# Kernel tuning notes

Measured on AMD Instinct MI355X. Metric: run time of the kernel, lower is better.

Reference implementation:

```python
import jax, jax.numpy as jnp
import numpy as np

B, C, N, Hdim, Wdim = 32, 64, 16384, 128, 128  # N = Hdim*Wdim, C = dim = num_embeddings
EPS = 1e-5


def setup_inputs() -> dict:
    key = jax.random.key(0)
    ks = jax.random.split(key, 6)
    s = 0.05  # weight scale
    return {
        "x": jax.random.normal(ks[0], (B, C, N), dtype=jnp.float32),
        "Wq": jax.random.normal(ks[1], (C, C), dtype=jnp.float32) * s,   # Conv1d q (1x1)
        "bq": jnp.zeros((C,), jnp.float32),
        "gamma": jnp.ones((C,), jnp.float32),                              # BatchNorm1d affine
        "beta": jnp.zeros((C,), jnp.float32),
        "Wq2": jax.random.normal(ks[2], (C, C), dtype=jnp.float32) * s,  # Conv1d q2 (1x1)
        "bq2": jnp.zeros((C,), jnp.float32),
        "Wsr": jax.random.normal(ks[3], (C, C), dtype=jnp.float32) * s,  # Conv2d sr, k=1,s=1 -> 1x1
        "bsr": jnp.zeros((C,), jnp.float32),
        "Wc": jax.random.normal(ks[4], (C, C), dtype=jnp.float32) * s,   # Conv1d conv (1x1, no bias)
        "H": Hdim,
        "W": Wdim,
    }


def reference(x, Wq, bq, gamma, beta, Wq2, bq2, Wsr, bsr, Wc, H, W):
    # x: (B, C, N), N = H*W, sr_ratio = 1
    # q = q2(BN(q(x))) -- all 1x1 convs; BN uses batch statistics (torch training mode)
    q = jnp.einsum('oc,bcn->bon', Wq, x) + bq[None, :, None]            # (B,C,N)
    mu = q.mean(axis=(0, 2), keepdims=True)
    var = q.var(axis=(0, 2), keepdims=True)
    q = (q - mu) * jax.lax.rsqrt(var + EPS)
    q = q * gamma[None, :, None] + beta[None, :, None]
    q = jnp.einsum('oc,bcn->bon', Wq2, q) + bq2[None, :, None]          # (B,C,N)

    # k = sr(x) with kernel/stride 1 -> 1x1 conv, then permute to (B,N,C)
    k = jnp.einsum('oc,bcn->bon', Wsr, x) + bsr[None, :, None]          # (B,C,N)

    # v = AvgPool1d(C) over the channel axis of x^T -> channel mean, (B,1,N)
    v = x.mean(axis=1, keepdims=True)                                    # (B,1,N)

    # attn = q @ k^T over the N axis -> (B,C,C), then MaxPool1d(C) -> row-wise max (B,C,1)
    attn = jnp.einsum('bcn,bdn->bcd', q, k)                              # (B,C,C)
    attn = attn.max(axis=-1, keepdims=True)                              # (B,C,1)

    # out = conv( attn @ v )  -- outer product broadcast, then 1x1 conv (no bias)
    out = attn * v                                                       # (B,C,N)
    out = jnp.einsum('oc,bcn->bon', Wc, out)                             # (B,C,N)
    return out
```

## Files before the change

### kernel.cpp

```cpp
#include <hip/hip_runtime.h>
#include <hip/hip_bf16.h>

#define B_ 32
#define C_ 64
#define N_ 16384
constexpr float BN_INV = 1.0f / (32.0f * 16384.0f);

typedef float f32x4 __attribute__((ext_vector_type(4)));
typedef short s16x8 __attribute__((ext_vector_type(8)));

constexpr size_t WS_GPART = 0;
constexpr size_t WS_RPART = WS_GPART + (size_t)512 * 4096;
constexpr size_t WS_G     = WS_RPART + (size_t)512 * 64;
constexpr size_t WS_RB    = WS_G + (size_t)32 * 4096;
constexpr size_t WS_V     = WS_RB + (size_t)32 * 64;
constexpr size_t WS_W     = WS_V + (size_t)32 * N_;

__device__ constexpr int P1I[10] = {0,0,0,0,1,1,1,2,2,3};
__device__ constexpr int P1J[10] = {0,1,2,3,1,2,3,2,3,3};
__device__ constexpr int P1AT[4][4] = {{0,1,2,3},{1,4,5,6},{2,5,7,8},{3,6,8,9}};

__device__ __forceinline__ unsigned short bf16_rne_s(float f) {
    unsigned u = __float_as_uint(f);
    unsigned r = u + 0x7FFFu + ((u >> 16) & 1u);
    return (unsigned short)(r >> 16);
}
__device__ __forceinline__ unsigned cvt_pk_bf16(float lo, float hi) {
    unsigned r;
    asm("v_cvt_pk_bf16_f32 %0, %1, %2" : "=v"(r) : "v"(lo), "v"(hi));
    return r;
}
__device__ __forceinline__ void cvt8hi(const f32x4& a, const f32x4& b, s16x8& hi) {
    union { unsigned w[4]; s16x8 v; } u;
    u.w[0] = cvt_pk_bf16(a[0], a[1]);
    u.w[1] = cvt_pk_bf16(a[2], a[3]);
    u.w[2] = cvt_pk_bf16(b[0], b[1]);
    u.w[3] = cvt_pk_bf16(b[2], b[3]);
    hi = u.v;
}

__global__ __launch_bounds__(512, 2) void k1(const float* __restrict__ x, float* __restrict__ ws) {
    __shared__ __align__(16) float rawb[4][10 * 256];
    __shared__ float rws[8][64];
    const int t = threadIdx.x, wv = t >> 6, lane = t & 63;
    const int b = blockIdx.x >> 4, ch = blockIdx.x & 15;
    const int kg = lane >> 4, cl = lane & 15;
    const float* xb = x + ((size_t)b * C_ + cl) * N_ + ch * 1024 + kg * 8;

    f32x4 accP1[10];
    #pragma unroll
    for (int i = 0; i < 10; ++i) accP1[i] = (f32x4){0.f, 0.f, 0.f, 0.f};
    f32x4 rs = {0.f, 0.f, 0.f, 0.f};

    f32x4 cA[4], cB[4], nA[4], nB[4];
    #pragma unroll
    for (int g = 0; g < 4; ++g) {
        cA[g] = *(const f32x4*)(xb + (size_t)g * (16 * N_) + wv * 32);
        cB[g] = *(const f32x4*)(xb + (size_t)g * (16 * N_) + wv * 32 + 4);
    }

    for (int w = 0; w < 4; ++w) {
        if (w < 3) {
            const int noff = (8 * (w + 1) + wv) * 32;
            #pragma unroll
            for (int g = 0; g < 4; ++g) {
                nA[g] = *(const f32x4*)(xb + (size_t)g * (16 * N_) + noff);
                nB[g] = *(const f32x4*)(xb + (size_t)g * (16 * N_) + noff + 4);
            }
        }
        s16x8 hi[4];
        #pragma unroll
        for (int g = 0; g < 4; ++g) cvt8hi(cA[g], cB[g], hi[g]);

        f32x4 s0 = cA[0] + cA[1] + cA[2] + cA[3];
        f32x4 s1 = cB[0] + cB[1] + cB[2] + cB[3];
        #pragma unroll
        for (int m = 1; m <= 8; m <<= 1) {
            #pragma unroll
            for (int j = 0; j < 4; ++j) {
                s0[j] += __shfl_xor(s0[j], m);
                s1[j] += __shfl_xor(s1[j], m);
            }
        }
        if (cl == 0) {
            float* vp = ws + WS_V + (size_t)b * N_ + ch * 1024 + (8 * w + wv) * 32 + kg * 8;
            *(f32x4*)vp       = s0 * 0.015625f;
            *(f32x4*)(vp + 4) = s1 * 0.015625f;
        }
        #pragma unroll
        for (int g = 0; g < 4; ++g)
            rs[g] += cA[g][0] + cA[g][1] + cA[g][2] + cA[g][3]
                   + cB[g][0] + cB[g][1] + cB[g][2] + cB[g][3];

        #pragma unroll
        for (int i = 0; i < 10; ++i)
            accP1[i] = __builtin_amdgcn_mfma_f32_16x16x32_bf16(hi[P1I[i]], hi[P1J[i]], accP1[i], 0, 0, 0);

        #pragma unroll
        for (int g = 0; g < 4; ++g) { cA[g] = nA[g]; cB[g] = nB[g]; }
    }

    #pragma unroll
    for (int g = 0; g < 4; ++g) {
        rs[g] += __shfl_xor(rs[g], 16);
        rs[g] += __shfl_xor(rs[g], 32);
    }
    if (lane < 16) {
        #pragma unroll
        for (int g = 0; g < 4; ++g) rws[wv][g * 16 + lane] = rs[g];
    }

    if (wv < 4) {
        float* dst = rawb[wv];
        #pragma unroll
        for (int i = 0; i < 10; ++i) *(f32x4*)(dst + i * 256 + lane * 4) = accP1[i];
    }
    __syncthreads();
    if (wv >= 4) {
        float* dst = rawb[wv - 4];
        #pragma unroll
        for (int i = 0; i < 10; ++i) {
            f32x4 o = *(f32x4*)(dst + i * 256 + lane * 4);
            *(f32x4*)(dst + i * 256 + lane * 4) = o + accP1[i];
        }
    }
    __syncthreads();
    if (t < 64) {
        float s = 0.f;
        #pragma unroll
        for (int g = 0; g < 8; ++g) s += rws[g][t];
        ws[WS_RPART + (size_t)blockIdx.x * 64 + t] = s;
    }
    float* gp = ws + WS_GPART + (size_t)blockIdx.x * 4096;
    for (int e = t; e < 4096; e += 512) {
        const int r = e >> 6, c = e & 63;
        const int bi = r >> 4, bj = c >> 4, rr = r & 15, cc = c & 15;
        const int i1 = P1AT[bi][bj] * 256;
        const int o1 = (bi <= bj) ? (((rr >> 2) * 16 + cc) * 4 + (rr & 3))
                                  : (((cc >> 2) * 16 + rr) * 4 + (cc & 3));
        gp[e] = rawb[0][i1 + o1] + rawb[1][i1 + o1] + rawb[2][i1 + o1] + rawb[3][i1 + o1];
    }
}

__global__ __launch_bounds__(256) void k2a(float* __restrict__ ws) {
    const int b = blockIdx.x >> 3, sl = blockIdx.x & 7, t = threadIdx.x;
    #pragma unroll
    for (int h = 0; h < 2; ++h) {
        const int e = sl * 512 + h * 256 + t;
        float s = 0.f;
        for (int chn = 0; chn < 16; ++chn) s += ws[WS_GPART + ((size_t)(b * 16 + chn)) * 4096 + e];
        ws[WS_G + (size_t)b * 4096 + e] = s;
    }
    if (sl == 0 && t < 64) {
        float s = 0.f;
        for (int chn = 0; chn < 16; ++chn) s += ws[WS_RPART + (size_t)(b * 16 + chn) * 64 + t];
        ws[WS_RB + b * 64 + t] = s;
    }
}

__global__ __launch_bounds__(256) void k2b(const float* __restrict__ Wq, const float* __restrict__ gamma,
                                           const float* __restrict__ beta, const float* __restrict__ Wq2,
                                           const float* __restrict__ bq2, const float* __restrict__ Wsr,
                                           const float* __restrict__ bsr, const float* __restrict__ Wc,
                                           float* __restrict__ ws) {
    __shared__ __align__(16) unsigned short OPH[3][64 * 72];
    __shared__ float F1[64 * 65], F2[64 * 65];
    __shared__ float mS[64], muS[64], DS[64], abv[64], quadS[64];
    __shared__ float rl[64], ul[64], avs[64], sbv[64], pls[64], aml[64];
    const int bb = blockIdx.x, t = threadIdx.x;
    const int w = t >> 6, lane = t & 63, cl = lane & 15, jg = lane >> 4;
    const int sr = t >> 2, sc0 = (t & 3) * 16;

    {
        f32x4 s[4];
        #pragma unroll
        for (int j = 0; j < 4; ++j) s[j] = (f32x4){0.f, 0.f, 0.f, 0.f};
        for (int b = 0; b < 32; ++b) {
            const float* gbp = ws + WS_G + (size_t)b * 4096 + sr * 64 + sc0;
            #pragma unroll
            for (int j = 0; j < 4; ++j) s[j] += *(const f32x4*)(gbp + 4 * j);
        }
        s16x8 h8[2];
        #pragma unroll
        for (int q = 0; q < 2; ++q)
            #pragma unroll
            for (int j = 0; j < 8; ++j)
                h8[q][j] = (short)bf16_rne_s(s[q * 2 + (j >> 2)][j & 3] * BN_INV);
        *(s16x8*)(&OPH[0][sr * 72 + sc0])     = h8[0];
        *(s16x8*)(&OPH[0][sr * 72 + sc0 + 8]) = h8[1];
    }
    #pragma unroll
    for (int mtx = 0; mtx < 2; ++mtx) {
        const float* src = (mtx == 0 ? Wq : Wq2) + sr * 64 + sc0;
        float* F = (mtx == 0) ? F1 : F2;
        s16x8 h8[2];
        #pragma unroll
        for (int q = 0; q < 2; ++q) {
            f32x4 a = *(const f32x4*)(src + q * 8);
            f32x4 b = *(const f32x4*)(src + q * 8 + 4);
            #pragma unroll
            for (int j = 0; j < 8; ++j) {
                float v = (j < 4) ? a[j] : b[j - 4];
                F[sr * 65 + sc0 + q * 8 + j] = v;
                h8[q][j] = (short)bf16_rne_s(v);
            }
        }
        unsigned short* H = OPH[1 + mtx];
        *(s16x8*)(&H[sr * 72 + sc0])     = h8[0];
        *(s16x8*)(&H[sr * 72 + sc0 + 8]) = h8[1];
    }
    if (t < 64) {
        float sm = 0.f;
        for (int b = 0; b < 32; ++b) sm += ws[WS_RB + b * 64 + t];
        mS[t] = sm * BN_INV;
        rl[t] = ws[WS_RB + bb * 64 + t];
        sbv[t] = bsr[t];
    }
    __syncthreads();

    auto mm64 = [&](const unsigned short* AH, const unsigned short* BH, f32x4 acc[4]) {
        #pragma unroll
        for (int ks = 0; ks < 2; ++ks) {
            const int ko = ks * 32 + jg * 8;
            s16x8 ah = *(const s16x8*)(AH + (16 * w + cl) * 72 + ko);
            #pragma unroll
            for (int bj = 0; bj < 4; ++bj) {
                s16x8 bh = *(const s16x8*)(BH + (16 * bj + cl) * 72 + ko);
                acc[bj] = __builtin_amdgcn_mfma_f32_16x16x32_bf16(ah, bh, acc[bj], 0, 0, 0);
            }
        }
    };

    {
        f32x4 acc[4];
        #pragma unroll
        for (int i = 0; i < 4; ++i) acc[i] = (f32x4){0.f, 0.f, 0.f, 0.f};
        mm64(OPH[1], OPH[0], acc);
        float s[4] = {0.f, 0.f, 0.f, 0.f};
        #pragma unroll
        for (int j = 0; j < 4; ++j) {
            const int row = 16 * w + jg * 4 + j;
            #pragma unroll
            for (int bj = 0; bj < 4; ++bj) s[j] += acc[bj][j] * F1[row * 65 + 16 * bj + cl];
        }
        #pragma unroll
        for (int m = 1; m <= 8; m <<= 1)
            #pragma unroll
            for (int j = 0; j < 4; ++j) s[j] += __shfl_xor(s[j], m);
        if (cl == 0) {
            #pragma unroll
            for (int j = 0; j < 4; ++j) quadS[16 * w + jg * 4 + j] = s[j];
        }
        if (t < 64) {
            float s2 = 0.f;
            for (int c = 0; c < 64; ++c) s2 += F1[t * 65 + c] * mS[c];
            muS[t] = s2;
        }
    }
    __syncthreads();

    if (t < 64) {
        const float var = quadS[t] - muS[t] * muS[t];
        const float D = gamma[t] * rsqrtf(var + 1e-5f);
        DS[t] = D;
        abv[t] = beta[t] - D * muS[t];
    }
    __syncthreads();
    {
        s16x8 h8[2];
        #pragma unroll
        for (int q = 0; q < 2; ++q)
            #pragma unroll
            for (int j = 0; j < 8; ++j) {
                const int c = sc0 + q * 8 + j;
                h8[q][j] = (short)bf16_rne_s(DS[c] * F1[c * 65 + sr]);
            }
        *(s16x8*)(&OPH[0][sr * 72 + sc0])     = h8[0];
        *(s16x8*)(&OPH[0][sr * 72 + sc0 + 8]) = h8[1];
    }
    if (t < 64) {
        float s = 0.f;
        for (int k = 0; k < 64; ++k) s += F2[t * 65 + k] * abv[k];
        avs[t] = s + bq2[t];
    }
    __syncthreads();

    {
        f32x4 acc[4];
        #pragma unroll
        for (int i = 0; i < 4; ++i) acc[i] = (f32x4){0.f, 0.f, 0.f, 0.f};
        mm64(OPH[2], OPH[0], acc);
        float s[4] = {0.f, 0.f, 0.f, 0.f};
        #pragma unroll
        for (int bj = 0; bj < 4; ++bj) {
            const float cv = rl[16 * bj + cl];
            #pragma unroll
            for (int j = 0; j < 4; ++j) s[j] += acc[bj][j] * cv;
        }
        #pragma unroll
        for (int m = 1; m <= 8; m <<= 1)
            #pragma unroll
            for (int j = 0; j < 4; ++j) s[j] += __shfl_xor(s[j], m);
        if (cl == 0) {
            #pragma unroll
            for (int j = 0; j < 4; ++j) ul[16 * w + jg * 4 + j] = s[j];
        }
        #pragma unroll
        for (int bj = 0; bj < 4; ++bj)
            #pragma unroll
            for (int j = 0; j < 4; ++j) {
                const int row = 16 * w + jg * 4 + j, col = 16 * bj + cl;
                OPH[1][row * 72 + col] = (unsigned short)bf16_rne_s(acc[bj][j]);
            }
    }
    __syncthreads();

    {
        const float* gbp = ws + WS_G + (size_t)bb * 4096 + sr * 64 + sc0;
        s16x8 h8[2];
        #pragma unroll
        for (int q = 0; q < 2; ++q) {
            f32x4 a = *(const f32x4*)(gbp + q * 8);
            f32x4 b = *(const f32x4*)(gbp + q * 8 + 4);
            #pragma unroll
            for (int j = 0; j < 8; ++j)
                h8[q][j] = (short)bf16_rne_s((j < 4) ? a[j] : b[j - 4]);
        }
        *(s16x8*)(&OPH[0][sr * 72 + sc0])     = h8[0];
        *(s16x8*)(&OPH[0][sr * 72 + sc0 + 8]) = h8[1];
        const float* ssrc = Wsr + sr * 64 + sc0;
        #pragma unroll
        for (int q = 0; q < 2; ++q) {
            f32x4 a = *(const f32x4*)(ssrc + q * 8);
            f32x4 b = *(const f32x4*)(ssrc + q * 8 + 4);
            #pragma unroll
            for (int j = 0; j < 8; ++j) {
                float v = (j < 4) ? a[j] : b[j - 4];
                F1[sr * 65 + sc0 + q * 8 + j] = v;
                h8[q][j] = (short)bf16_rne_s(v);
            }
        }
        *(s16x8*)(&OPH[2][sr * 72 + sc0])     = h8[0];
        *(s16x8*)(&OPH[2][sr * 72 + sc0 + 8]) = h8[1];
    }
    __syncthreads();

    f32x4 accT[4];
    #pragma unroll
    for (int i = 0; i < 4; ++i) accT[i] = (f32x4){0.f, 0.f, 0.f, 0.f};
    if (t < 64) {
        float s = 0.f;
        for (int k = 0; k < 64; ++k) s += F1[t * 65 + k] * rl[k];
        pls[t] = s + 16384.f * sbv[t];
    }
    mm64(OPH[1], OPH[0], accT);
    __syncthreads();
    #pragma unroll
    for (int bj = 0; bj < 4; ++bj)
        #pragma unroll
        for (int j = 0; j < 4; ++j) {
            const int row = 16 * w + jg * 4 + j, col = 16 * bj + cl;
            OPH[0][row * 72 + col] = (unsigned short)bf16_rne_s(accT[bj][j]);
        }
    __syncthreads();

    {
        f32x4 acc[4];
        #pragma unroll
        for (int i = 0; i < 4; ++i) acc[i] = (f32x4){0.f, 0.f, 0.f, 0.f};
        mm64(OPH[0], OPH[2], acc);
        float mx[4] = {-3.4e38f, -3.4e38f, -3.4e38f, -3.4e38f};
        #pragma unroll
        for (int j = 0; j < 4; ++j) {
            const int row = 16 * w + jg * 4 + j;
            const float ur = ul[row], ar = avs[row];
            #pragma unroll
            for (int bj = 0; bj < 4; ++bj) {
                const int col = 16 * bj + cl;
                const float v = acc[bj][j] + ur * sbv[col] + ar * pls[col];
                mx[j] = fmaxf(mx[j], v);
            }
        }
        #pragma unroll
        for (int m = 1; m <= 8; m <<= 1)
            #pragma unroll
            for (int j = 0; j < 4; ++j) mx[j] = fmaxf(mx[j], __shfl_xor(mx[j], m));
        if (cl == 0) {
            #pragma unroll
            for (int j = 0; j < 4; ++j) aml[16 * w + jg * 4 + j] = mx[j];
        }
    }
    __syncthreads();

    if (t < 64) {
        float s = 0.f;
        for (int c = 0; c < 64; ++c) s += Wc[t * 64 + c] * aml[c];
        ws[WS_W + bb * 64 + t] = s;
    }
}

__global__ __launch_bounds__(256) void k3(const float* __restrict__ ws, float* __restrict__ out) {
    const int blk = blockIdx.x;
    const int b = blk >> 6, seg = blk & 63;
    const int r0 = (seg >> 4) * 16, chk = seg & 15;
    __shared__ float wls[16];
    const int t = threadIdx.x;
    if (t < 16) wls[t] = ws[WS_W + b * 64 + r0 + t];
    __syncthreads();
    const size_t nb = (size_t)chk * 1024 + 4 * t;
    const f32x4 v4 = *(const f32x4*)(ws + WS_V + (size_t)b * N_ + nb);
    float* ob = out + ((size_t)b * C_ + r0) * N_ + nb;
    #pragma unroll
    for (int o = 0; o < 16; ++o) {
        __builtin_nontemporal_store(v4 * wls[o], (f32x4*)(ob + (size_t)o * N_));
    }
}

extern "C" void kernel_launch(void* const* d_in, const int* in_sizes, int n_in,
                              void* d_out, int out_size, void* d_ws, size_t ws_size,
                              hipStream_t stream) {
    const float* x     = (const float*)d_in[0];
    const float* Wq    = (const float*)d_in[1];
    const float* gamma = (const float*)d_in[3];
    const float* beta  = (const float*)d_in[4];
    const float* Wq2   = (const float*)d_in[5];
    const float* bq2   = (const float*)d_in[6];
    const float* Wsr   = (const float*)d_in[7];
    const float* bsr   = (const float*)d_in[8];
    const float* Wc    = (const float*)d_in[9];
    float* ws  = (float*)d_ws;
    float* out = (float*)d_out;

    hipLaunchKernelGGL(k1,  dim3(512),  dim3(512), 0, stream, x, ws);
    hipLaunchKernelGGL(k2a, dim3(256),  dim3(256), 0, stream, ws);
    hipLaunchKernelGGL(k2b, dim3(32),   dim3(256), 0, stream,
                       Wq, gamma, beta, Wq2, bq2, Wsr, bsr, Wc, ws);
    hipLaunchKernelGGL(k3,  dim3(2048), dim3(256), 0, stream, ws, out);
}
```

Before: 74.97 us.

## Split batch-independent BN/Q-projection work into single-block kernel before per-batch stage

The per-batch k2b kernel, which recomputed the batch-independent BN statistics and the folded Wq2·diag(D)·Wq matrix in each of its 32 blocks, is split in two. A single-block k2s computes the shared A matrix and bias vector once and writes them to workspace. A 32-block k2c then does only the per-batch work, which also reorders the u/p vector computations to overlap with the MFMA. This removes redundant work across blocks but adds a kernel launch and a serial single-block stage, and some vectors now use bf16-rounded weights.

New measurement: 79.62 us. 1.06x slower.

```diff
diff --git a/kernel.cpp b/kernel.cpp
--- a/kernel.cpp
+++ b/kernel.cpp
@@ -14,7 +14,9 @@
 constexpr size_t WS_G     = WS_RPART + (size_t)512 * 64;
 constexpr size_t WS_RB    = WS_G + (size_t)32 * 4096;
 constexpr size_t WS_V     = WS_RB + (size_t)32 * 64;
-constexpr size_t WS_W     = WS_V + (size_t)32 * N_;
+constexpr size_t WS_A     = WS_V + (size_t)32 * N_;
+constexpr size_t WS_AVEC  = WS_A + 4096;
+constexpr size_t WS_W     = WS_AVEC + 64;
 
 __device__ constexpr int P1I[10] = {0,0,0,0,1,1,1,2,2,3};
 __device__ constexpr int P1J[10] = {0,1,2,3,1,2,3,2,3,3};
@@ -24,6 +26,9 @@
     unsigned u = __float_as_uint(f);
     unsigned r = u + 0x7FFFu + ((u >> 16) & 1u);
     return (unsigned short)(r >> 16);
+}
+__device__ __forceinline__ float bf16f(unsigned short u) {
+    return __uint_as_float(((unsigned)u) << 16);
 }
 __device__ __forceinline__ unsigned cvt_pk_bf16(float lo, float hi) {
     unsigned r;
@@ -158,16 +163,13 @@
     }
 }
 
-__global__ __launch_bounds__(256) void k2b(const float* __restrict__ Wq, const float* __restrict__ gamma,
+__global__ __launch_bounds__(256) void k2s(const float* __restrict__ Wq, const float* __restrict__ gamma,
                                            const float* __restrict__ beta, const float* __restrict__ Wq2,
-                                           const float* __restrict__ bq2, const float* __restrict__ Wsr,
-                                           const float* __restrict__ bsr, const float* __restrict__ Wc,
-                                           float* __restrict__ ws) {
-    __shared__ __align__(16) unsigned short OPH[3][64 * 72];
-    __shared__ float F1[64 * 65], F2[64 * 65];
+                                           const float* __restrict__ bq2, float* __restrict__ ws) {
+    __shared__ __align__(16) unsigned short OPH0[64 * 72], OPH1[64 * 72], OPH2[64 * 72];
+    __shared__ float F1[64 * 65];
     __shared__ float mS[64], muS[64], DS[64], abv[64], quadS[64];
-    __shared__ float rl[64], ul[64], avs[64], sbv[64], pls[64], aml[64];
-    const int bb = blockIdx.x, t = threadIdx.x;
+    const int t = threadIdx.x;
     const int w = t >> 6, lane = t & 63, cl = lane & 15, jg = lane >> 4;
     const int sr = t >> 2, sc0 = (t & 3) * 16;
 
@@ -175,6 +177,7 @@
         f32x4 s[4];
         #pragma unroll
         for (int j = 0; j < 4; ++j) s[j] = (f32x4){0.f, 0.f, 0.f, 0.f};
+        #pragma unroll 4
         for (int b = 0; b < 32; ++b) {
             const float* gbp = ws + WS_G + (size_t)b * 4096 + sr * 64 + sc0;
             #pragma unroll
@@ -186,13 +189,11 @@
             #pragma unroll
             for (int j = 0; j < 8; ++j)
                 h8[q][j] = (short)bf16_rne_s(s[q * 2 + (j >> 2)][j & 3] * BN_INV);
-        *(s16x8*)(&OPH[0][sr * 72 + sc0])     = h8[0];
-        *(s16x8*)(&OPH[0][sr * 72 + sc0 + 8]) = h8[1];
-    }
-    #pragma unroll
-    for (int mtx = 0; mtx < 2; ++mtx) {
-        const float* src = (mtx == 0 ? Wq : Wq2) + sr * 64 + sc0;
-        float* F = (mtx == 0) ? F1 : F2;
+        *(s16x8*)(&OPH0[sr * 72 + sc0])     = h8[0];
+        *(s16x8*)(&OPH0[sr * 72 + sc0 + 8]) = h8[1];
+    }
+    {
+        const float* src = Wq + sr * 64 + sc0;
         s16x8 h8[2];
         #pragma unroll
         for (int q = 0; q < 2; ++q) {
@@ -201,20 +202,32 @@
             #pragma unroll
             for (int j = 0; j < 8; ++j) {
                 float v = (j < 4) ? a[j] : b[j - 4];
-                F[sr * 65 + sc0 + q * 8 + j] = v;
+                F1[sr * 65 + sc0 + q * 8 + j] = v;
                 h8[q][j] = (short)bf16_rne_s(v);
             }
         }
-        unsigned short* H = OPH[1 + mtx];
-        *(s16x8*)(&H[sr * 72 + sc0])     = h8[0];
-        *(s16x8*)(&H[sr * 72 + sc0 + 8]) = h8[1];
+        *(s16x8*)(&OPH1[sr * 72 + sc0])     = h8[0];
+        *(s16x8*)(&OPH1[sr * 72 + sc0 + 8]) = h8[1];
+    }
+    {
+        const float* src = Wq2 + sr * 64 + sc0;
+        s16x8 h8[2];
+        #pragma unroll
+        for (int q = 0; q < 2; ++q) {
+            f32x4 a = *(const f32x4*)(src + q * 8);
+            f32x4 b = *(const f32x4*)(src + q * 8 + 4);
+            #pragma unroll
+            for (int j = 0; j < 8; ++j)
+                h8[q][j] = (short)bf16_rne_s((j < 4) ? a[j] : b[j - 4]);
+        }
+        *(s16x8*)(&OPH2[sr * 72 + sc0])     = h8[0];
+        *(s16x8*)(&OPH2[sr * 72 + sc0 + 8]) = h8[1];
     }
     if (t < 64) {
         float sm = 0.f;
+        #pragma unroll 8
         for (int b = 0; b < 32; ++b) sm += ws[WS_RB + b * 64 + t];
         mS[t] = sm * BN_INV;
-        rl[t] = ws[WS_RB + bb * 64 + t];
-        sbv[t] = bsr[t];
     }
     __syncthreads();
 
@@ -235,7 +248,7 @@
         f32x4 acc[4];
         #pragma unroll
         for (int i = 0; i < 4; ++i) acc[i] = (f32x4){0.f, 0.f, 0.f, 0.f};
-        mm64(OPH[1], OPH[0], acc);
+        mm64(OPH1, OPH0, acc);
         float s[4] = {0.f, 0.f, 0.f, 0.f};
         #pragma unroll
         for (int j = 0; j < 4; ++j) {
@@ -253,6 +266,7 @@
         }
         if (t < 64) {
             float s2 = 0.f;
+            #pragma unroll 8
             for (int c = 0; c < 64; ++c) s2 += F1[t * 65 + c] * mS[c];
             muS[t] = s2;
         }
@@ -275,13 +289,14 @@
                 const int c = sc0 + q * 8 + j;
                 h8[q][j] = (short)bf16_rne_s(DS[c] * F1[c * 65 + sr]);
             }
-        *(s16x8*)(&OPH[0][sr * 72 + sc0])     = h8[0];
-        *(s16x8*)(&OPH[0][sr * 72 + sc0 + 8]) = h8[1];
+        *(s16x8*)(&OPH0[sr * 72 + sc0])     = h8[0];
+        *(s16x8*)(&OPH0[sr * 72 + sc0 + 8]) = h8[1];
     }
     if (t < 64) {
         float s = 0.f;
-        for (int k = 0; k < 64; ++k) s += F2[t * 65 + k] * abv[k];
-        avs[t] = s + bq2[t];
+        #pragma unroll 8
+        for (int k = 0; k < 64; ++k) s += bf16f(OPH2[t * 72 + k]) * abv[k];
+        ws[WS_AVEC + t] = s + bq2[t];
     }
     __syncthreads();
 
@@ -289,86 +304,106 @@
         f32x4 acc[4];
         #pragma unroll
         for (int i = 0; i < 4; ++i) acc[i] = (f32x4){0.f, 0.f, 0.f, 0.f};
-        mm64(OPH[2], OPH[0], acc);
-        float s[4] = {0.f, 0.f, 0.f, 0.f};
-        #pragma unroll
-        for (int bj = 0; bj < 4; ++bj) {
-            const float cv = rl[16 * bj + cl];
-            #pragma unroll
-            for (int j = 0; j < 4; ++j) s[j] += acc[bj][j] * cv;
-        }
-        #pragma unroll
-        for (int m = 1; m <= 8; m <<= 1)
-            #pragma unroll
-            for (int j = 0; j < 4; ++j) s[j] += __shfl_xor(s[j], m);
-        if (cl == 0) {
-            #pragma unroll
-            for (int j = 0; j < 4; ++j) ul[16 * w + jg * 4 + j] = s[j];
-        }
+        mm64(OPH2, OPH0, acc);
         #pragma unroll
         for (int bj = 0; bj < 4; ++bj)
             #pragma unroll
             for (int j = 0; j < 4; ++j) {
                 const int row = 16 * w + jg * 4 + j, col = 16 * bj + cl;
-                OPH[1][row * 72 + col] = (unsigned short)bf16_rne_s(acc[bj][j]);
-            }
-    }
-    __syncthreads();
-
-    {
-        const float* gbp = ws + WS_G + (size_t)bb * 4096 + sr * 64 + sc0;
-        s16x8 h8[2];
-        #pragma unroll
-        for (int q = 0; q < 2; ++q) {
-            f32x4 a = *(const f32x4*)(gbp + q * 8);
-            f32x4 b = *(const f32x4*)(gbp + q * 8 + 4);
-            #pragma unroll
-            for (int j = 0; j < 8; ++j)
-                h8[q][j] = (short)bf16_rne_s((j < 4) ? a[j] : b[j - 4]);
-        }
-        *(s16x8*)(&OPH[0][sr * 72 + sc0])     = h8[0];
-        *(s16x8*)(&OPH[0][sr * 72 + sc0 + 8]) = h8[1];
+                ws[WS_A + row * 64 + col] = acc[bj][j];
+            }
+    }
+}
+
+__global__ __launch_bounds__(256) void k2c(const float* __restrict__ Wsr, const float* __restrict__ bsr,
+                                           const float* __restrict__ Wc, float* __restrict__ ws) {
+    __shared__ __align__(16) unsigned short OPA[64 * 72], OPG[64 * 72], OPS[64 * 72], OPT[64 * 72];
+    __shared__ float rl[64], avs[64], sbv[64], ul[64], pls[64], aml[64];
+    const int bb = blockIdx.x, t = threadIdx.x;
+    const int w = t >> 6, lane = t & 63, cl = lane & 15, jg = lane >> 4;
+    const int sr = t >> 2, sc0 = (t & 3) * 16;
+
+    {
+        const float* asrc = ws + WS_A + sr * 64 + sc0;
+        const float* gsrc = ws + WS_G + (size_t)bb * 4096 + sr * 64 + sc0;
         const float* ssrc = Wsr + sr * 64 + sc0;
-        #pragma unroll
-        for (int q = 0; q < 2; ++q) {
-            f32x4 a = *(const f32x4*)(ssrc + q * 8);
-            f32x4 b = *(const f32x4*)(ssrc + q * 8 + 4);
+        f32x4 av[4], gv[4], sv[4];
+        #pragma unroll
+        for (int j = 0; j < 4; ++j) {
+            av[j] = *(const f32x4*)(asrc + 4 * j);
+            gv[j] = *(const f32x4*)(gsrc + 4 * j);
+            sv[j] = *(const f32x4*)(ssrc + 4 * j);
+        }
+        s16x8 ha[2], hg[2], hs[2];
+        #pragma unroll
+        for (int q = 0; q < 2; ++q)
             #pragma unroll
             for (int j = 0; j < 8; ++j) {
-                float v = (j < 4) ? a[j] : b[j - 4];
-                F1[sr * 65 + sc0 + q * 8 + j] = v;
-                h8[q][j] = (short)bf16_rne_s(v);
-            }
-        }
-        *(s16x8*)(&OPH[2][sr * 72 + sc0])     = h8[0];
-        *(s16x8*)(&OPH[2][sr * 72 + sc0 + 8]) = h8[1];
-    }
-    __syncthreads();
-
-    f32x4 accT[4];
-    #pragma unroll
-    for (int i = 0; i < 4; ++i) accT[i] = (f32x4){0.f, 0.f, 0.f, 0.f};
-    if (t < 64) {
-        float s = 0.f;
-        for (int k = 0; k < 64; ++k) s += F1[t * 65 + k] * rl[k];
-        pls[t] = s + 16384.f * sbv[t];
-    }
-    mm64(OPH[1], OPH[0], accT);
-    __syncthreads();
-    #pragma unroll
-    for (int bj = 0; bj < 4; ++bj)
-        #pragma unroll
-        for (int j = 0; j < 4; ++j) {
-            const int row = 16 * w + jg * 4 + j, col = 16 * bj + cl;
-            OPH[0][row * 72 + col] = (unsigned short)bf16_rne_s(accT[bj][j]);
-        }
+                const int ji = q * 2 + (j >> 2), jj = j & 3;
+                ha[q][j] = (short)bf16_rne_s(av[ji][jj]);
+                hg[q][j] = (short)bf16_rne_s(gv[ji][jj]);
+                hs[q][j] = (short)bf16_rne_s(sv[ji][jj]);
+            }
+        *(s16x8*)(&OPA[sr * 72 + sc0])     = ha[0];
+        *(s16x8*)(&OPA[sr * 72 + sc0 + 8]) = ha[1];
+        *(s16x8*)(&OPG[sr * 72 + sc0])     = hg[0];
+        *(s16x8*)(&OPG[sr * 72 + sc0 + 8]) = hg[1];
+        *(s16x8*)(&OPS[sr * 72 + sc0])     = hs[0];
+        *(s16x8*)(&OPS[sr * 72 + sc0 + 8]) = hs[1];
+    }
+    if (t < 64) {
+        rl[t]  = ws[WS_RB + bb * 64 + t];
+        avs[t] = ws[WS_AVEC + t];
+        sbv[t] = bsr[t];
+    }
+    __syncthreads();
+
+    auto mm64 = [&](const unsigned short* AH, const unsigned short* BH, f32x4 acc[4]) {
+        #pragma unroll
+        for (int ks = 0; ks < 2; ++ks) {
+            const int ko = ks * 32 + jg * 8;
+            s16x8 ah = *(const s16x8*)(AH + (16 * w + cl) * 72 + ko);
+            #pragma unroll
+            for (int bj = 0; bj < 4; ++bj) {
+                s16x8 bh = *(const s16x8*)(BH + (16 * bj + cl) * 72 + ko);
+                acc[bj] = __builtin_amdgcn_mfma_f32_16x16x32_bf16(ah, bh, acc[bj], 0, 0, 0);
+            }
+        }
+    };
+
+    {
+        f32x4 accT[4];
+        #pragma unroll
+        for (int i = 0; i < 4; ++i) accT[i] = (f32x4){0.f, 0.f, 0.f, 0.f};
+        mm64(OPA, OPG, accT);
+        if (w == 1) {
+            const int d = t - 64;
+            float s = 0.f;
+            #pragma unroll 8
+            for (int k = 0; k < 64; ++k) s += bf16f(OPA[d * 72 + k]) * rl[k];
+            ul[d] = s;
+        } else if (w == 2) {
+            const int d = t - 128;
+            float s = 0.f;
+            #pragma unroll 8
+            for (int k = 0; k < 64; ++k) s += bf16f(OPS[d * 72 + k]) * rl[k];
+            pls[d] = s + 16384.f * sbv[d];
+        }
+        #pragma unroll
+        for (int bj = 0; bj < 4; ++bj)
+            #pragma unroll
+            for (int j = 0; j < 4; ++j) {
+                const int row = 16 * w + jg * 4 + j, col = 16 * bj + cl;
+                OPT[row * 72 + col] = (unsigned short)bf16_rne_s(accT[bj][j]);
+            }
+    }
     __syncthreads();
 
     {
         f32x4 acc[4];
         #pragma unroll
         for (int i = 0; i < 4; ++i) acc[i] = (f32x4){0.f, 0.f, 0.f, 0.f};
-        mm64(OPH[0], OPH[2], acc);
+        mm64(OPT, OPS, acc);
         float mx[4] = {-3.4e38f, -3.4e38f, -3.4e38f, -3.4e38f};
         #pragma unroll
         for (int j = 0; j < 4; ++j) {
@@ -394,6 +429,7 @@
 
     if (t < 64) {
         float s = 0.f;
+        #pragma unroll 8
         for (int c = 0; c < 64; ++c) s += Wc[t * 64 + c] * aml[c];
         ws[WS_W + bb * 64 + t] = s;
     }
@@ -433,7 +469,7 @@
 
     hipLaunchKernelGGL(k1,  dim3(512),  dim3(512), 0, stream, x, ws);
     hipLaunchKernelGGL(k2a, dim3(256),  dim3(256), 0, stream, ws);
-    hipLaunchKernelGGL(k2b, dim3(32),   dim3(256), 0, stream,
-                       Wq, gamma, beta, Wq2, bq2, Wsr, bsr, Wc, ws);
+    hipLaunchKernelGGL(k2s, dim3(1),    dim3(256), 0, stream, Wq, gamma, beta, Wq2, bq2, ws);
+    hipLaunchKernelGGL(k2c, dim3(32),   dim3(256), 0, stream, Wsr, bsr, Wc, ws);
     hipLaunchKernelGGL(k3,  dim3(2048), dim3(256), 0, stream, ws, out);
 }
```

## Precompute batch Gram sum via atomics and reassociate per-batch attention matmuls in k2b

Applied to the files above, without the earlier changes.

k2a now atomically accumulates the cross-batch Gram and row sums into new workspace slots, zeroed by k1 block 0. This removes the 32-way redundant reduction that every k2b block used to perform. k2b loads all five operand matrices into bf16 shared tiles up front and splits warps so the BN-statistics matmul and the Wsr·G product run concurrently. It also reorders the chain so the final attention matmul uses the precomputed Wsr·G, and it drops the fp32 weight copies in favour of bf16 reads. The risks are float atomic ordering nondeterminism and slightly reduced precision, since the weights are now rounded to bf16 in the scalar dot products.

Result: faster. 68.91 us (-8.1%).

```diff
diff --git a/kernel.cpp b/kernel.cpp
--- a/kernel.cpp
+++ b/kernel.cpp
@@ -15,6 +15,8 @@
 constexpr size_t WS_RB    = WS_G + (size_t)32 * 4096;
 constexpr size_t WS_V     = WS_RB + (size_t)32 * 64;
 constexpr size_t WS_W     = WS_V + (size_t)32 * N_;
+constexpr size_t WS_GBAR  = WS_W + (size_t)32 * 64;
+constexpr size_t WS_MBAR  = WS_GBAR + 4096;
 
 __device__ constexpr int P1I[10] = {0,0,0,0,1,1,1,2,2,3};
 __device__ constexpr int P1J[10] = {0,1,2,3,1,2,3,2,3,3};
@@ -24,6 +26,9 @@
     unsigned u = __float_as_uint(f);
     unsigned r = u + 0x7FFFu + ((u >> 16) & 1u);
     return (unsigned short)(r >> 16);
+}
+__device__ __forceinline__ float bf16f(unsigned short u) {
+    return __uint_as_float(((unsigned)u) << 16);
 }
 __device__ __forceinline__ unsigned cvt_pk_bf16(float lo, float hi) {
     unsigned r;
@@ -46,6 +51,12 @@
     const int b = blockIdx.x >> 4, ch = blockIdx.x & 15;
     const int kg = lane >> 4, cl = lane & 15;
     const float* xb = x + ((size_t)b * C_ + cl) * N_ + ch * 1024 + kg * 8;
+
+    if (blockIdx.x == 0) {
+        #pragma unroll
+        for (int i = 0; i < 8; ++i) ws[WS_GBAR + t * 8 + i] = 0.f;
+        if (t < 64) ws[WS_MBAR + t] = 0.f;
+    }
 
     f32x4 accP1[10];
     #pragma unroll
@@ -150,11 +161,13 @@
         float s = 0.f;
         for (int chn = 0; chn < 16; ++chn) s += ws[WS_GPART + ((size_t)(b * 16 + chn)) * 4096 + e];
         ws[WS_G + (size_t)b * 4096 + e] = s;
+        unsafeAtomicAdd(ws + WS_GBAR + e, s);
     }
     if (sl == 0 && t < 64) {
         float s = 0.f;
         for (int chn = 0; chn < 16; ++chn) s += ws[WS_RPART + (size_t)(b * 16 + chn) * 64 + t];
         ws[WS_RB + b * 64 + t] = s;
+        unsafeAtomicAdd(ws + WS_MBAR + t, s);
     }
 }
 
@@ -163,66 +176,44 @@
                                            const float* __restrict__ bq2, const float* __restrict__ Wsr,
                                            const float* __restrict__ bsr, const float* __restrict__ Wc,
                                            float* __restrict__ ws) {
-    __shared__ __align__(16) unsigned short OPH[3][64 * 72];
-    __shared__ float F1[64 * 65], F2[64 * 65];
-    __shared__ float mS[64], muS[64], DS[64], abv[64], quadS[64];
+    __shared__ __align__(16) unsigned short OPH[6][64 * 72];
+    __shared__ float quadS[64], muS[64], DS[64], abv[64], mS[64];
     __shared__ float rl[64], ul[64], avs[64], sbv[64], pls[64], aml[64];
     const int bb = blockIdx.x, t = threadIdx.x;
     const int w = t >> 6, lane = t & 63, cl = lane & 15, jg = lane >> 4;
     const int sr = t >> 2, sc0 = (t & 3) * 16;
 
     {
-        f32x4 s[4];
-        #pragma unroll
-        for (int j = 0; j < 4; ++j) s[j] = (f32x4){0.f, 0.f, 0.f, 0.f};
-        for (int b = 0; b < 32; ++b) {
-            const float* gbp = ws + WS_G + (size_t)b * 4096 + sr * 64 + sc0;
-            #pragma unroll
-            for (int j = 0; j < 4; ++j) s[j] += *(const f32x4*)(gbp + 4 * j);
-        }
-        s16x8 h8[2];
-        #pragma unroll
-        for (int q = 0; q < 2; ++q)
-            #pragma unroll
-            for (int j = 0; j < 8; ++j)
-                h8[q][j] = (short)bf16_rne_s(s[q * 2 + (j >> 2)][j & 3] * BN_INV);
-        *(s16x8*)(&OPH[0][sr * 72 + sc0])     = h8[0];
-        *(s16x8*)(&OPH[0][sr * 72 + sc0 + 8]) = h8[1];
-    }
-    #pragma unroll
-    for (int mtx = 0; mtx < 2; ++mtx) {
-        const float* src = (mtx == 0 ? Wq : Wq2) + sr * 64 + sc0;
-        float* F = (mtx == 0) ? F1 : F2;
-        s16x8 h8[2];
-        #pragma unroll
-        for (int q = 0; q < 2; ++q) {
-            f32x4 a = *(const f32x4*)(src + q * 8);
-            f32x4 b = *(const f32x4*)(src + q * 8 + 4);
-            #pragma unroll
-            for (int j = 0; j < 8; ++j) {
-                float v = (j < 4) ? a[j] : b[j - 4];
-                F[sr * 65 + sc0 + q * 8 + j] = v;
-                h8[q][j] = (short)bf16_rne_s(v);
-            }
-        }
-        unsigned short* H = OPH[1 + mtx];
-        *(s16x8*)(&H[sr * 72 + sc0])     = h8[0];
-        *(s16x8*)(&H[sr * 72 + sc0 + 8]) = h8[1];
+        const float* srcs[5] = { ws + WS_GBAR, Wq, Wq2, ws + WS_G + (size_t)bb * 4096, Wsr };
+        #pragma unroll
+        for (int mI = 0; mI < 5; ++mI) {
+            const float sc = (mI == 0) ? BN_INV : 1.f;
+            const float* src = srcs[mI] + sr * 64 + sc0;
+            s16x8 h8[2];
+            #pragma unroll
+            for (int q = 0; q < 2; ++q) {
+                f32x4 a = *(const f32x4*)(src + q * 8);
+                f32x4 b2 = *(const f32x4*)(src + q * 8 + 4);
+                #pragma unroll
+                for (int j = 0; j < 8; ++j)
+                    h8[q][j] = (short)bf16_rne_s(((j < 4) ? a[j] : b2[j - 4]) * sc);
+            }
+            *(s16x8*)(&OPH[mI][sr * 72 + sc0])     = h8[0];
+            *(s16x8*)(&OPH[mI][sr * 72 + sc0 + 8]) = h8[1];
+        }
     }
     if (t < 64) {
-        float sm = 0.f;
-        for (int b = 0; b < 32; ++b) sm += ws[WS_RB + b * 64 + t];
-        mS[t] = sm * BN_INV;
-        rl[t] = ws[WS_RB + bb * 64 + t];
+        mS[t]  = ws[WS_MBAR + t] * BN_INV;
+        rl[t]  = ws[WS_RB + bb * 64 + t];
         sbv[t] = bsr[t];
     }
     __syncthreads();
 
-    auto mm64 = [&](const unsigned short* AH, const unsigned short* BH, f32x4 acc[4]) {
+    auto mmStripe = [&](const unsigned short* AH, const unsigned short* BH, int row0, f32x4* acc) {
         #pragma unroll
         for (int ks = 0; ks < 2; ++ks) {
             const int ko = ks * 32 + jg * 8;
-            s16x8 ah = *(const s16x8*)(AH + (16 * w + cl) * 72 + ko);
+            s16x8 ah = *(const s16x8*)(AH + (row0 + cl) * 72 + ko);
             #pragma unroll
             for (int bj = 0; bj < 4; ++bj) {
                 s16x8 bh = *(const s16x8*)(BH + (16 * bj + cl) * 72 + ko);
@@ -231,30 +222,63 @@
         }
     };
 
-    {
-        f32x4 acc[4];
-        #pragma unroll
-        for (int i = 0; i < 4; ++i) acc[i] = (f32x4){0.f, 0.f, 0.f, 0.f};
-        mm64(OPH[1], OPH[0], acc);
-        float s[4] = {0.f, 0.f, 0.f, 0.f};
-        #pragma unroll
-        for (int j = 0; j < 4; ++j) {
-            const int row = 16 * w + jg * 4 + j;
-            #pragma unroll
-            for (int bj = 0; bj < 4; ++bj) s[j] += acc[bj][j] * F1[row * 65 + 16 * bj + cl];
-        }
-        #pragma unroll
-        for (int m = 1; m <= 8; m <<= 1)
-            #pragma unroll
-            for (int j = 0; j < 4; ++j) s[j] += __shfl_xor(s[j], m);
-        if (cl == 0) {
-            #pragma unroll
-            for (int j = 0; j < 4; ++j) quadS[16 * w + jg * 4 + j] = s[j];
+    if (w < 2) {
+        f32x4 acc2[2][4];
+        #pragma unroll
+        for (int st = 0; st < 2; ++st)
+            #pragma unroll
+            for (int i = 0; i < 4; ++i) acc2[st][i] = (f32x4){0.f, 0.f, 0.f, 0.f};
+        mmStripe(OPH[1], OPH[0], 32 * w,      acc2[0]);
+        mmStripe(OPH[1], OPH[0], 32 * w + 16, acc2[1]);
+        #pragma unroll
+        for (int st = 0; st < 2; ++st) {
+            float s[4] = {0.f, 0.f, 0.f, 0.f};
+            #pragma unroll
+            for (int j = 0; j < 4; ++j) {
+                const int row = 32 * w + 16 * st + jg * 4 + j;
+                #pragma unroll
+                for (int bj = 0; bj < 4; ++bj)
+                    s[j] += acc2[st][bj][j] * bf16f(OPH[1][row * 72 + 16 * bj + cl]);
+            }
+            #pragma unroll
+            for (int m = 1; m <= 8; m <<= 1)
+                #pragma unroll
+                for (int j = 0; j < 4; ++j) s[j] += __shfl_xor(s[j], m);
+            if (cl == 0) {
+                #pragma unroll
+                for (int j = 0; j < 4; ++j) quadS[32 * w + 16 * st + jg * 4 + j] = s[j];
+            }
         }
         if (t < 64) {
             float s2 = 0.f;
-            for (int c = 0; c < 64; ++c) s2 += F1[t * 65 + c] * mS[c];
+            #pragma unroll 8
+            for (int c = 0; c < 64; ++c) s2 += bf16f(OPH[1][t * 72 + c]) * mS[c];
             muS[t] = s2;
+        }
+    } else {
+        const int w2 = w - 2;
+        f32x4 acc2[2][4];
+        #pragma unroll
+        for (int st = 0; st < 2; ++st)
+            #pragma unroll
+            for (int i = 0; i < 4; ++i) acc2[st][i] = (f32x4){0.f, 0.f, 0.f, 0.f};
+        mmStripe(OPH[4], OPH[3], 32 * w2,      acc2[0]);
+        mmStripe(OPH[4], OPH[3], 32 * w2 + 16, acc2[1]);
+        #pragma unroll
+        for (int st = 0; st < 2; ++st)
+            #pragma unroll
+            for (int bj = 0; bj < 4; ++bj)
+                #pragma unroll
+                for (int j = 0; j < 4; ++j) {
+                    const int row = 32 * w2 + 16 * st + jg * 4 + j, col = 16 * bj + cl;
+                    OPH[5][row * 72 + col] = (unsigned short)bf16_rne_s(acc2[st][bj][j]);
+                }
+        const int t2 = t - 128;
+        if (t2 < 64) {
+            float s = 0.f;
+            #pragma unroll 8
+            for (int k = 0; k < 64; ++k) s += bf16f(OPH[4][t2 * 72 + k]) * rl[k];
+            pls[t2] = s + 16384.f * sbv[t2];
         }
     }
     __syncthreads();
@@ -267,21 +291,52 @@
     }
     __syncthreads();
     {
-        s16x8 h8[2];
-        #pragma unroll
-        for (int q = 0; q < 2; ++q)
+        #pragma unroll
+        for (int q = 0; q < 2; ++q) {
+            s16x8 h8;
             #pragma unroll
             for (int j = 0; j < 8; ++j) {
                 const int c = sc0 + q * 8 + j;
-                h8[q][j] = (short)bf16_rne_s(DS[c] * F1[c * 65 + sr]);
-            }
-        *(s16x8*)(&OPH[0][sr * 72 + sc0])     = h8[0];
-        *(s16x8*)(&OPH[0][sr * 72 + sc0 + 8]) = h8[1];
+                h8[j] = (short)bf16_rne_s(DS[c] * bf16f(OPH[1][c * 72 + sr]));
+            }
+            *(s16x8*)(&OPH[0][sr * 72 + sc0 + q * 8]) = h8;
+        }
     }
     if (t < 64) {
         float s = 0.f;
-        for (int k = 0; k < 64; ++k) s += F2[t * 65 + k] * abv[k];
+        #pragma unroll 8
+        for (int k = 0; k < 64; ++k) s += bf16f(OPH[2][t * 72 + k]) * abv[k];
         avs[t] = s + bq2[t];
+    }
+    __syncthreads();
+
+    {
+        f32x4 accA[4];
+        #pragma unroll
+        for (int i = 0; i < 4; ++i) accA[i] = (f32x4){0.f, 0.f, 0.f, 0.f};
+        mmStripe(OPH[2], OPH[0], 16 * w, accA);
+        float su[4] = {0.f, 0.f, 0.f, 0.f};
+        #pragma unroll
+        for (int bj = 0; bj < 4; ++bj) {
+            const float cv = rl[16 * bj + cl];
+            #pragma unroll
+            for (int j = 0; j < 4; ++j) su[j] += accA[bj][j] * cv;
+        }
+        #pragma unroll
+        for (int m = 1; m <= 8; m <<= 1)
+            #pragma unroll
+            for (int j = 0; j < 4; ++j) su[j] += __shfl_xor(su[j], m);
+        if (cl == 0) {
+            #pragma unroll
+            for (int j = 0; j < 4; ++j) ul[16 * w + jg * 4 + j] = su[j];
+        }
+        #pragma unroll
+        for (int bj = 0; bj < 4; ++bj)
+            #pragma unroll
+            for (int j = 0; j < 4; ++j) {
+                const int row = 16 * w + jg * 4 + j, col = 16 * bj + cl;
+                OPH[1][row * 72 + col] = (unsigned short)bf16_rne_s(accA[bj][j]);
+            }
     }
     __syncthreads();
 
@@ -289,86 +344,7 @@
         f32x4 acc[4];
         #pragma unroll
         for (int i = 0; i < 4; ++i) acc[i] = (f32x4){0.f, 0.f, 0.f, 0.f};
-        mm64(OPH[2], OPH[0], acc);
-        float s[4] = {0.f, 0.f, 0.f, 0.f};
-        #pragma unroll
-        for (int bj = 0; bj < 4; ++bj) {
-            const float cv = rl[16 * bj + cl];
-            #pragma unroll
-            for (int j = 0; j < 4; ++j) s[j] += acc[bj][j] * cv;
-        }
-        #pragma unroll
-        for (int m = 1; m <= 8; m <<= 1)
-            #pragma unroll
-            for (int j = 0; j < 4; ++j) s[j] += __shfl_xor(s[j], m);
-        if (cl == 0) {
-            #pragma unroll
-            for (int j = 0; j < 4; ++j) ul[16 * w + jg * 4 + j] = s[j];
-        }
-        #pragma unroll
-        for (int bj = 0; bj < 4; ++bj)
-            #pragma unroll
-            for (int j = 0; j < 4; ++j) {
-                const int row = 16 * w + jg * 4 + j, col = 16 * bj + cl;
-                OPH[1][row * 72 + col] = (unsigned short)bf16_rne_s(acc[bj][j]);
-            }
-    }
-    __syncthreads();
-
-    {
-        const float* gbp = ws + WS_G + (size_t)bb * 4096 + sr * 64 + sc0;
-        s16x8 h8[2];
-        #pragma unroll
-        for (int q = 0; q < 2; ++q) {
-            f32x4 a = *(const f32x4*)(gbp + q * 8);
-            f32x4 b = *(const f32x4*)(gbp + q * 8 + 4);
-            #pragma unroll
-            for (int j = 0; j < 8; ++j)
-                h8[q][j] = (short)bf16_rne_s((j < 4) ? a[j] : b[j - 4]);
-        }
-        *(s16x8*)(&OPH[0][sr * 72 + sc0])     = h8[0];
-        *(s16x8*)(&OPH[0][sr * 72 + sc0 + 8]) = h8[1];
-        const float* ssrc = Wsr + sr * 64 + sc0;
-        #pragma unroll
-        for (int q = 0; q < 2; ++q) {
-            f32x4 a = *(const f32x4*)(ssrc + q * 8);
-            f32x4 b = *(const f32x4*)(ssrc + q * 8 + 4);
-            #pragma unroll
-            for (int j = 0; j < 8; ++j) {
-                float v = (j < 4) ? a[j] : b[j - 4];
-                F1[sr * 65 + sc0 + q * 8 + j] = v;
-                h8[q][j] = (short)bf16_rne_s(v);
-            }
-        }
-        *(s16x8*)(&OPH[2][sr * 72 + sc0])     = h8[0];
-        *(s16x8*)(&OPH[2][sr * 72 + sc0 + 8]) = h8[1];
-    }
-    __syncthreads();
-
-    f32x4 accT[4];
-    #pragma unroll
-    for (int i = 0; i < 4; ++i) accT[i] = (f32x4){0.f, 0.f, 0.f, 0.f};
-    if (t < 64) {
-        float s = 0.f;
-        for (int k = 0; k < 64; ++k) s += F1[t * 65 + k] * rl[k];
-        pls[t] = s + 16384.f * sbv[t];
-    }
-    mm64(OPH[1], OPH[0], accT);
-    __syncthreads();
-    #pragma unroll
-    for (int bj = 0; bj < 4; ++bj)
-        #pragma unroll
-        for (int j = 0; j < 4; ++j) {
-            const int row = 16 * w + jg * 4 + j, col = 16 * bj + cl;
-            OPH[0][row * 72 + col] = (unsigned short)bf16_rne_s(accT[bj][j]);
-        }
-    __syncthreads();
-
-    {
-        f32x4 acc[4];
-        #pragma unroll
-        for (int i = 0; i < 4; ++i) acc[i] = (f32x4){0.f, 0.f, 0.f, 0.f};
-        mm64(OPH[0], OPH[2], acc);
+        mmStripe(OPH[1], OPH[5], 16 * w, acc);
         float mx[4] = {-3.4e38f, -3.4e38f, -3.4e38f, -3.4e38f};
         #pragma unroll
         for (int j = 0; j < 4; ++j) {
@@ -394,6 +370,7 @@
 
     if (t < 64) {
         float s = 0.f;
+        #pragma unroll 8
         for (int c = 0; c < 64; ++c) s += Wc[t * 64 + c] * aml[c];
         ws[WS_W + bb * 64 + t] = s;
     }
```
